# Kernel tuning notes

Hardware: AMD Instinct MI355X
Metric: run time of the kernel (lower is better)

The kernel has to match this reference:

```python
import jax, jax.numpy as jnp
import numpy as np

N_NODES = 50000
N_EDGES = 800000
IN_DIM = 64
EDGE_DIM = 32
OUT_DIM = 64
HID = IN_DIM + EDGE_DIM  # repo MLP defaults hidden width = layer input width


def setup_inputs() -> dict:
    key = jax.random.key(0)
    ks = jax.random.split(key, 7)
    x = jax.random.normal(ks[0], (N_NODES, IN_DIM), dtype=jnp.float32)
    edge_index = jax.random.randint(ks[1], (2, N_EDGES), 0, N_NODES, dtype=jnp.int64)
    edge_attr = jax.random.normal(ks[2], (N_EDGES, EDGE_DIM), dtype=jnp.float32)
    s1 = 1.0 / np.sqrt(HID)
    s2 = 1.0 / np.sqrt(HID)
    W1 = jax.random.normal(ks[3], (HID, HID), dtype=jnp.float32) * s1
    b1 = jnp.zeros((HID,), dtype=jnp.float32)
    W2 = jax.random.normal(ks[4], (HID, OUT_DIM), dtype=jnp.float32) * s2
    b2 = jnp.zeros((OUT_DIM,), dtype=jnp.float32)
    return {"x": x, "edge_index": edge_index, "edge_attr": edge_attr,
            "W1": W1, "b1": b1, "W2": W2, "b2": b2}


def reference(x, edge_index, edge_attr, W1, b1, W2, b2):
    row, col = edge_index[0], edge_index[1]
    n_nodes = x.shape[0]
    # gather source node features and fuse with edge features: [E, IN+EDGE]
    h = jnp.concatenate([x[row], edge_attr], axis=1)
    # MLP: one hidden layer with ReLU, linear output
    h = jax.nn.relu(h @ W1 + b1)
    h = h @ W2 + b2  # [E, OUT_DIM]
    # scatter_mean over destination (col) indices
    summed = jax.ops.segment_sum(h, col, num_segments=n_nodes)  # [N, OUT_DIM]
    counts = jax.ops.segment_sum(jnp.ones((h.shape[0],), dtype=h.dtype), col,
                                 num_segments=n_nodes)
    return summed / jnp.maximum(counts, 1.0)[:, None]
```

## Files before the change

### kernel.cpp

```cpp
#include <hip/hip_runtime.h>

#define N_EDGES  800000
#define N_NODES  50000
#define IN_DIM   64
#define EDGE_DIM 32
#define HID      96
#define OUT_DIM  64
#define BE       128
#define PAD      104
#define NTILES   (N_EDGES / BE)
#define THREADS  512
#define GRID     512
#define SCAN_B   1024
#define SCAN_NB  ((N_NODES + SCAN_B - 1) / SCAN_B)

typedef __attribute__((ext_vector_type(8))) short  short8;
typedef __attribute__((ext_vector_type(4))) ushort bf16x4;
typedef __attribute__((ext_vector_type(4))) float  f32x4;

__device__ inline ushort f2bf(float f) {
    union { float f; unsigned u; } v; v.f = f;
    unsigned r = v.u + 0x7FFFu + ((v.u >> 16) & 1u);
    return (ushort)(r >> 16);
}
__device__ inline float b2f(ushort u) {
    union { unsigned u; float f; } v; v.u = ((unsigned)u) << 16;
    return v.f;
}

__global__ __launch_bounds__(256) void zero_hist_kernel(int* __restrict__ hist) {
    int i = blockIdx.x * 256 + threadIdx.x;
    if (i < N_NODES) hist[i] = 0;
}

__global__ __launch_bounds__(256) void hist_kernel(const int* __restrict__ ei,
                                                   int* __restrict__ hist) {
    int e = blockIdx.x * 256 + threadIdx.x;
    if (e < N_EDGES) atomicAdd(&hist[ei[N_EDGES + e]], 1);
}

__global__ __launch_bounds__(SCAN_B) void scan1_kernel(const int* __restrict__ hist,
                                                       int* __restrict__ starts,
                                                       int* __restrict__ bsums) {
    __shared__ int buf[2][SCAN_B];
    const int tid = threadIdx.x;
    const int gid = blockIdx.x * SCAN_B + tid;
    int v = (gid < N_NODES) ? hist[gid] : 0;
    int cur = 0;
    buf[0][tid] = v;
    __syncthreads();
    #pragma unroll
    for (int off = 1; off < SCAN_B; off <<= 1) {
        int t = buf[cur][tid] + ((tid >= off) ? buf[cur][tid - off] : 0);
        buf[cur ^ 1][tid] = t;
        __syncthreads();
        cur ^= 1;
    }
    int incl = buf[cur][tid];
    if (gid < N_NODES) starts[gid] = incl;
    if (tid == SCAN_B - 1) bsums[blockIdx.x] = incl;
}

__global__ __launch_bounds__(64) void scan2_kernel(int* __restrict__ bsums) {
    if (threadIdx.x == 0) {
        int acc = 0;
        for (int i = 0; i < SCAN_NB; ++i) { int t = bsums[i]; bsums[i] = acc; acc += t; }
    }
}

__global__ __launch_bounds__(SCAN_B) void scan3_kernel(const int* __restrict__ hist,
                                                       int* __restrict__ starts,
                                                       int* __restrict__ cursor,
                                                       const int* __restrict__ bsums) {
    const int gid = blockIdx.x * SCAN_B + threadIdx.x;
    if (gid < N_NODES) {
        int e = starts[gid] - hist[gid] + bsums[blockIdx.x];
        starts[gid] = e;
        cursor[gid] = e;
    }
}

__global__ __launch_bounds__(256) void fill_kernel(const int* __restrict__ ei,
                                                   int* __restrict__ cursor,
                                                   int* __restrict__ ids) {
    int e = blockIdx.x * 256 + threadIdx.x;
    if (e < N_EDGES) {
        int c = ei[N_EDGES + e];
        int p = atomicAdd(&cursor[c], 1);
        ids[p] = e;
    }
}

__global__ __launch_bounds__(256) void zero_kernel(float* __restrict__ out,
                                                   float* __restrict__ cnt) {
    int i = blockIdx.x * 256 + threadIdx.x;
    if (i < N_NODES * OUT_DIM) out[i] = 0.0f;
    if (i < N_NODES) cnt[i] = 0.0f;
}

__global__ __launch_bounds__(256) void div_kernel(float* __restrict__ out,
                                                  const float* __restrict__ cnt) {
    int i = blockIdx.x * 256 + threadIdx.x;
    if (i < N_NODES * OUT_DIM) {
        float c = cnt[i / OUT_DIM];
        out[i] = out[i] / fmaxf(c, 1.0f);
    }
}

template <bool ATOMIC>
__global__ __launch_bounds__(THREADS, 4) void edge_mlp_mfma_kernel(
    const float* __restrict__ x,
    const int*   __restrict__ ei,
    const float* __restrict__ ea,
    const float* __restrict__ W1,
    const float* __restrict__ b1,
    const float* __restrict__ W2,
    const float* __restrict__ b2,
    float*       __restrict__ out,
    float*       __restrict__ cnt,
    ushort*      __restrict__ temp)
{
    __shared__ ushort sA[BE][PAD];
    __shared__ ushort sW1T[HID][PAD];
    __shared__ ushort sW2T[OUT_DIM][PAD];

    const int tid  = threadIdx.x;
    const int wave = tid >> 6;
    const int lane = tid & 63;
    const int lr   = lane & 15;
    const int lg   = lane >> 4;
    const int el_base = wave * 16;

    #pragma unroll 2
    for (int i = tid; i < HID * HID / 4; i += THREADS) {
        float4 v = reinterpret_cast<const float4*>(W1)[i];
        int k = (i * 4) / HID, n = (i * 4) % HID;
        sW1T[n + 0][k] = f2bf(v.x); sW1T[n + 1][k] = f2bf(v.y);
        sW1T[n + 2][k] = f2bf(v.z); sW1T[n + 3][k] = f2bf(v.w);
    }
    #pragma unroll 2
    for (int i = tid; i < HID * OUT_DIM / 4; i += THREADS) {
        float4 v = reinterpret_cast<const float4*>(W2)[i];
        int k = (i * 4) / OUT_DIM, n = (i * 4) % OUT_DIM;
        sW2T[n + 0][k] = f2bf(v.x); sW2T[n + 1][k] = f2bf(v.y);
        sW2T[n + 2][k] = f2bf(v.z); sW2T[n + 3][k] = f2bf(v.w);
    }
    float rb1[6], rb2[4];
    #pragma unroll
    for (int nt = 0; nt < 6; ++nt) rb1[nt] = b1[nt * 16 + lr];
    #pragma unroll
    for (int nt = 0; nt < 4; ++nt) rb2[nt] = b2[nt * 16 + lr];
    __syncthreads();

    for (int tl = blockIdx.x; tl < NTILES; tl += gridDim.x) {
        const int e0 = tl * BE;

        {
            const int el   = el_base + (lane >> 2);
            const int part = lane & 3;
            const int e    = e0 + el;
            const int src  = ei[e];
            const float4* xp = reinterpret_cast<const float4*>(x) + (size_t)src * 16;
            const float4* ep = reinterpret_cast<const float4*>(ea) + (size_t)e * 8;
            #pragma unroll
            for (int i = 0; i < 6; ++i) {
                const int f = part + 4 * i;
                float4 v = (i < 4) ? xp[f] : ep[f - 16];
                bf16x4 w = { f2bf(v.x), f2bf(v.y), f2bf(v.z), f2bf(v.w) };
                *(bf16x4*)&sA[el][f * 4] = w;
            }
            if constexpr (ATOMIC) {
                if (part == 0) atomicAdd(cnt + ei[N_EDGES + e], 1.0f);
            }
        }
        asm volatile("s_waitcnt lgkmcnt(0)" ::: "memory");
        __builtin_amdgcn_sched_barrier(0);

        short8 af[3];
        #pragma unroll
        for (int ks = 0; ks < 3; ++ks)
            af[ks] = *(const short8*)&sA[el_base + lr][ks * 32 + lg * 8];

        f32x4 acc1[6];
        #pragma unroll
        for (int nt = 0; nt < 6; ++nt) {
            float bv = rb1[nt];
            acc1[nt] = f32x4{ bv, bv, bv, bv };
        }
        #pragma unroll
        for (int nt = 0; nt < 6; ++nt) {
            short8 bf[3];
            #pragma unroll
            for (int ks = 0; ks < 3; ++ks)
                bf[ks] = *(const short8*)&sW1T[nt * 16 + lr][ks * 32 + lg * 8];
            #pragma unroll
            for (int ks = 0; ks < 3; ++ks)
                acc1[nt] = __builtin_amdgcn_mfma_f32_16x16x32_bf16(
                    af[ks], bf[ks], acc1[nt], 0, 0, 0);
        }

        #pragma unroll
        for (int nt = 0; nt < 6; ++nt)
            #pragma unroll
            for (int j = 0; j < 4; ++j)
                sA[el_base + lg * 4 + j][nt * 16 + lr] =
                    f2bf(fmaxf(acc1[nt][j], 0.0f));
        asm volatile("s_waitcnt lgkmcnt(0)" ::: "memory");
        __builtin_amdgcn_sched_barrier(0);

        short8 a2[3];
        #pragma unroll
        for (int ks = 0; ks < 3; ++ks)
            a2[ks] = *(const short8*)&sA[el_base + lr][ks * 32 + lg * 8];

        f32x4 acc2[4];
        #pragma unroll
        for (int nt = 0; nt < 4; ++nt) {
            float bv = rb2[nt];
            acc2[nt] = f32x4{ bv, bv, bv, bv };
        }
        #pragma unroll
        for (int nt = 0; nt < 4; ++nt) {
            short8 bf[3];
            #pragma unroll
            for (int ks = 0; ks < 3; ++ks)
                bf[ks] = *(const short8*)&sW2T[nt * 16 + lr][ks * 32 + lg * 8];
            #pragma unroll
            for (int ks = 0; ks < 3; ++ks)
                acc2[nt] = __builtin_amdgcn_mfma_f32_16x16x32_bf16(
                    a2[ks], bf[ks], acc2[nt], 0, 0, 0);
        }

        if constexpr (ATOMIC) {
            int nd[4];
            #pragma unroll
            for (int j = 0; j < 4; ++j)
                nd[j] = ei[N_EDGES + e0 + el_base + lg * 4 + j];
            #pragma unroll
            for (int nt = 0; nt < 4; ++nt)
                #pragma unroll
                for (int j = 0; j < 4; ++j)
                    atomicAdd(out + (size_t)nd[j] * OUT_DIM + nt * 16 + lr,
                              acc2[nt][j]);
        } else {
            #pragma unroll
            for (int nt = 0; nt < 4; ++nt)
                #pragma unroll
                for (int j = 0; j < 4; ++j)
                    sA[el_base + lg * 4 + j][nt * 16 + lr] = f2bf(acc2[nt][j]);
            asm volatile("s_waitcnt lgkmcnt(0)" ::: "memory");
            __builtin_amdgcn_sched_barrier(0);
            const int rr = lane >> 2, pp = lane & 3;
            ushort* dst = temp + (size_t)(e0 + el_base + rr) * OUT_DIM + pp * 16;
            short8 v0 = *(const short8*)&sA[el_base + rr][pp * 16];
            short8 v1 = *(const short8*)&sA[el_base + rr][pp * 16 + 8];
            *(short8*)dst = v0;
            *(short8*)(dst + 8) = v1;
        }
    }
}

__global__ __launch_bounds__(256) void pull_kernel(const ushort* __restrict__ temp,
                                                   const int* __restrict__ ids,
                                                   const int* __restrict__ starts,
                                                   const int* __restrict__ hist,
                                                   float* __restrict__ out) {
    const int wave = threadIdx.x >> 6;
    const int lane = threadIdx.x & 63;
    const int node = blockIdx.x * 4 + wave;
    if (node >= N_NODES) return;
    const int deg = hist[node];
    const int st  = starts[node];
    float s = 0.0f;
    int i = 0;
    for (; i + 4 <= deg; i += 4) {
        int e0 = ids[st + i], e1 = ids[st + i + 1];
        int e2 = ids[st + i + 2], e3 = ids[st + i + 3];
        float a = b2f(temp[(size_t)e0 * OUT_DIM + lane]);
        float b = b2f(temp[(size_t)e1 * OUT_DIM + lane]);
        float c = b2f(temp[(size_t)e2 * OUT_DIM + lane]);
        float d = b2f(temp[(size_t)e3 * OUT_DIM + lane]);
        s += (a + b) + (c + d);
    }
    for (; i < deg; ++i)
        s += b2f(temp[(size_t)ids[st + i] * OUT_DIM + lane]);
    out[(size_t)node * OUT_DIM + lane] = s / fmaxf((float)deg, 1.0f);
}

extern "C" void kernel_launch(void* const* d_in, const int* in_sizes, int n_in,
                              void* d_out, int out_size, void* d_ws, size_t ws_size,
                              hipStream_t stream) {
    const float* x  = (const float*)d_in[0];
    const int*   ei = (const int*)d_in[1];
    const float* ea = (const float*)d_in[2];
    const float* W1 = (const float*)d_in[3];
    const float* b1 = (const float*)d_in[4];
    const float* W2 = (const float*)d_in[5];
    const float* b2 = (const float*)d_in[6];
    float* out = (float*)d_out;

    char* ws = (char*)d_ws;
    const size_t tempB    = (size_t)N_EDGES * OUT_DIM * sizeof(ushort);
    const size_t idsOff   = tempB;
    const size_t histOff  = idsOff + (size_t)N_EDGES * 4;
    const size_t strOff   = histOff + (size_t)N_NODES * 4;
    const size_t curOff   = strOff + (size_t)N_NODES * 4;
    const size_t bsumOff  = curOff + (size_t)N_NODES * 4;
    const size_t need     = bsumOff + 64 * 4;

    if (ws_size >= need) {
        ushort* temp  = (ushort*)ws;
        int* ids      = (int*)(ws + idsOff);
        int* hist     = (int*)(ws + histOff);
        int* starts   = (int*)(ws + strOff);
        int* cursor   = (int*)(ws + curOff);
        int* bsums    = (int*)(ws + bsumOff);

        zero_hist_kernel<<<(N_NODES + 255) / 256, 256, 0, stream>>>(hist);
        hist_kernel<<<N_EDGES / 256, 256, 0, stream>>>(ei, hist);
        scan1_kernel<<<SCAN_NB, SCAN_B, 0, stream>>>(hist, starts, bsums);
        scan2_kernel<<<1, 64, 0, stream>>>(bsums);
        scan3_kernel<<<SCAN_NB, SCAN_B, 0, stream>>>(hist, starts, cursor, bsums);
        fill_kernel<<<N_EDGES / 256, 256, 0, stream>>>(ei, cursor, ids);
        edge_mlp_mfma_kernel<false><<<GRID, THREADS, 0, stream>>>(
            x, ei, ea, W1, b1, W2, b2, out, nullptr, temp);
        pull_kernel<<<(N_NODES + 3) / 4, 256, 0, stream>>>(temp, ids, starts, hist, out);
    } else {
        float* cnt = (float*)d_ws;
        zero_kernel<<<(N_NODES * OUT_DIM + 255) / 256, 256, 0, stream>>>(out, cnt);
        edge_mlp_mfma_kernel<true><<<GRID, THREADS, 0, stream>>>(
            x, ei, ea, W1, b1, W2, b2, out, cnt, nullptr);
        div_kernel<<<(N_NODES * OUT_DIM + 255) / 256, 256, 0, stream>>>(out, cnt);
    }
}
```

Measured before the change: 204.0 us.

## Process edges in destination-sorted order and fuse segmented reduction into MLP kernel

The fill kernel now writes edges into CSR order as source, edge-id and destination arrays. The MLP kernel processes edges in that order and reduces runs of equal destinations within each 16-row wave tile before issuing float atomics into the output. This removes the bf16 temp buffer round-trip and the separate pull kernel, but adds atomics, a memset of the output and a divide pass. It also folds the bsums scan into scan3 with a wave reduction, replaces the zeroing kernel with memsets, and keeps the W2 fragments in registers across tiles.

After: 250.7 us. 1.23x slower.

```diff
diff --git a/kernel.cpp b/kernel.cpp
--- a/kernel.cpp
+++ b/kernel.cpp
@@ -28,11 +28,6 @@
     return v.f;
 }
 
-__global__ __launch_bounds__(256) void zero_hist_kernel(int* __restrict__ hist) {
-    int i = blockIdx.x * 256 + threadIdx.x;
-    if (i < N_NODES) hist[i] = 0;
-}
-
 __global__ __launch_bounds__(256) void hist_kernel(const int* __restrict__ ei,
                                                    int* __restrict__ hist) {
     int e = blockIdx.x * 256 + threadIdx.x;
@@ -61,20 +56,21 @@
     if (tid == SCAN_B - 1) bsums[blockIdx.x] = incl;
 }
 
-__global__ __launch_bounds__(64) void scan2_kernel(int* __restrict__ bsums) {
-    if (threadIdx.x == 0) {
-        int acc = 0;
-        for (int i = 0; i < SCAN_NB; ++i) { int t = bsums[i]; bsums[i] = acc; acc += t; }
-    }
-}
-
 __global__ __launch_bounds__(SCAN_B) void scan3_kernel(const int* __restrict__ hist,
                                                        int* __restrict__ starts,
                                                        int* __restrict__ cursor,
                                                        const int* __restrict__ bsums) {
+    __shared__ int s_off;
+    if (threadIdx.x < 64) {
+        int v = ((int)threadIdx.x < (int)blockIdx.x) ? bsums[threadIdx.x] : 0;
+        #pragma unroll
+        for (int o = 32; o >= 1; o >>= 1) v += __shfl_xor(v, o, 64);
+        if (threadIdx.x == 0) s_off = v;
+    }
+    __syncthreads();
     const int gid = blockIdx.x * SCAN_B + threadIdx.x;
     if (gid < N_NODES) {
-        int e = starts[gid] - hist[gid] + bsums[blockIdx.x];
+        int e = starts[gid] - hist[gid] + s_off;
         starts[gid] = e;
         cursor[gid] = e;
     }
@@ -82,12 +78,16 @@
 
 __global__ __launch_bounds__(256) void fill_kernel(const int* __restrict__ ei,
                                                    int* __restrict__ cursor,
-                                                   int* __restrict__ ids) {
+                                                   int* __restrict__ srcs,
+                                                   int* __restrict__ eids,
+                                                   int* __restrict__ dsts) {
     int e = blockIdx.x * 256 + threadIdx.x;
     if (e < N_EDGES) {
         int c = ei[N_EDGES + e];
         int p = atomicAdd(&cursor[c], 1);
-        ids[p] = e;
+        srcs[p] = ei[e];
+        eids[p] = e;
+        dsts[p] = c;
     }
 }
 
@@ -107,8 +107,164 @@
     }
 }
 
-template <bool ATOMIC>
-__global__ __launch_bounds__(THREADS, 4) void edge_mlp_mfma_kernel(
+__global__ __launch_bounds__(256) void div_int_kernel(float* __restrict__ out,
+                                                      const int* __restrict__ hist) {
+    int i = blockIdx.x * 256 + threadIdx.x;
+    if (i < N_NODES * OUT_DIM) {
+        float c = (float)hist[i >> 6];
+        out[i] = out[i] / fmaxf(c, 1.0f);
+    }
+}
+
+__global__ __launch_bounds__(THREADS, 4) void edge_mlp_csr_kernel(
+    const float* __restrict__ x,
+    const float* __restrict__ ea,
+    const int*   __restrict__ srcs,
+    const int*   __restrict__ eids,
+    const int*   __restrict__ dsts,
+    const float* __restrict__ W1,
+    const float* __restrict__ b1,
+    const float* __restrict__ W2,
+    const float* __restrict__ b2,
+    float*       __restrict__ out)
+{
+    __shared__ ushort sA[BE][PAD];
+    __shared__ ushort sW1T[HID][PAD];
+    __shared__ ushort sW2T[OUT_DIM][PAD];
+
+    const int tid  = threadIdx.x;
+    const int wave = tid >> 6;
+    const int lane = tid & 63;
+    const int lr   = lane & 15;
+    const int lg   = lane >> 4;
+    const int el_base = wave * 16;
+    const int el   = el_base + (lane >> 2);
+    const int part = lane & 3;
+
+    #pragma unroll 2
+    for (int i = tid; i < HID * HID / 4; i += THREADS) {
+        float4 v = reinterpret_cast<const float4*>(W1)[i];
+        int k = (i * 4) / HID, n = (i * 4) % HID;
+        sW1T[n + 0][k] = f2bf(v.x); sW1T[n + 1][k] = f2bf(v.y);
+        sW1T[n + 2][k] = f2bf(v.z); sW1T[n + 3][k] = f2bf(v.w);
+    }
+    #pragma unroll 2
+    for (int i = tid; i < HID * OUT_DIM / 4; i += THREADS) {
+        float4 v = reinterpret_cast<const float4*>(W2)[i];
+        int k = (i * 4) / OUT_DIM, n = (i * 4) % OUT_DIM;
+        sW2T[n + 0][k] = f2bf(v.x); sW2T[n + 1][k] = f2bf(v.y);
+        sW2T[n + 2][k] = f2bf(v.z); sW2T[n + 3][k] = f2bf(v.w);
+    }
+    float rb1[6], rb2[4];
+    #pragma unroll
+    for (int nt = 0; nt < 6; ++nt) rb1[nt] = b1[nt * 16 + lr];
+    #pragma unroll
+    for (int nt = 0; nt < 4; ++nt) rb2[nt] = b2[nt * 16 + lr];
+    __syncthreads();
+
+    short8 bw2[4][3];
+    #pragma unroll
+    for (int nt = 0; nt < 4; ++nt)
+        #pragma unroll
+        for (int ks = 0; ks < 3; ++ks)
+            bw2[nt][ks] = *(const short8*)&sW2T[nt * 16 + lr][ks * 32 + lg * 8];
+
+    for (int tl = blockIdx.x; tl < NTILES; tl += GRID) {
+        const int e0 = tl * BE;
+
+        {
+            const int slot = e0 + el;
+            const int src  = srcs[slot];
+            const int eid  = eids[slot];
+            const float4* xp = reinterpret_cast<const float4*>(x) + (size_t)src * 16;
+            const float4* ep = reinterpret_cast<const float4*>(ea) + (size_t)eid * 8;
+            #pragma unroll
+            for (int i = 0; i < 6; ++i) {
+                const int f = part + 4 * i;
+                float4 v = (i < 4) ? xp[f] : ep[f - 16];
+                bf16x4 w = { f2bf(v.x), f2bf(v.y), f2bf(v.z), f2bf(v.w) };
+                *(bf16x4*)&sA[el][f * 4] = w;
+            }
+        }
+        int dreg[17];
+        #pragma unroll
+        for (int r = 0; r < 16; ++r) dreg[r] = dsts[e0 + el_base + r];
+        dreg[16] = -1;
+
+        asm volatile("s_waitcnt lgkmcnt(0)" ::: "memory");
+        __builtin_amdgcn_sched_barrier(0);
+
+        short8 af[3];
+        #pragma unroll
+        for (int ks = 0; ks < 3; ++ks)
+            af[ks] = *(const short8*)&sA[el_base + lr][ks * 32 + lg * 8];
+
+        f32x4 acc1[6];
+        #pragma unroll
+        for (int nt = 0; nt < 6; ++nt) {
+            float bv = rb1[nt];
+            acc1[nt] = f32x4{ bv, bv, bv, bv };
+        }
+        #pragma unroll
+        for (int nt = 0; nt < 6; ++nt) {
+            short8 bf[3];
+            #pragma unroll
+            for (int ks = 0; ks < 3; ++ks)
+                bf[ks] = *(const short8*)&sW1T[nt * 16 + lr][ks * 32 + lg * 8];
+            #pragma unroll
+            for (int ks = 0; ks < 3; ++ks)
+                acc1[nt] = __builtin_amdgcn_mfma_f32_16x16x32_bf16(
+                    af[ks], bf[ks], acc1[nt], 0, 0, 0);
+        }
+
+        #pragma unroll
+        for (int nt = 0; nt < 6; ++nt)
+            #pragma unroll
+            for (int j = 0; j < 4; ++j)
+                sA[el_base + lg * 4 + j][nt * 16 + lr] =
+                    f2bf(fmaxf(acc1[nt][j], 0.0f));
+        asm volatile("s_waitcnt lgkmcnt(0)" ::: "memory");
+        __builtin_amdgcn_sched_barrier(0);
+
+        short8 a2[3];
+        #pragma unroll
+        for (int ks = 0; ks < 3; ++ks)
+            a2[ks] = *(const short8*)&sA[el_base + lr][ks * 32 + lg * 8];
+
+        f32x4 acc2[4];
+        #pragma unroll
+        for (int nt = 0; nt < 4; ++nt) {
+            float bv = rb2[nt];
+            acc2[nt] = f32x4{ bv, bv, bv, bv };
+        }
+        #pragma unroll
+        for (int nt = 0; nt < 4; ++nt)
+            #pragma unroll
+            for (int ks = 0; ks < 3; ++ks)
+                acc2[nt] = __builtin_amdgcn_mfma_f32_16x16x32_bf16(
+                    a2[ks], bw2[nt][ks], acc2[nt], 0, 0, 0);
+
+        #pragma unroll
+        for (int nt = 0; nt < 4; ++nt)
+            #pragma unroll
+            for (int j = 0; j < 4; ++j)
+                sA[el_base + lg * 4 + j][nt * 16 + lr] = f2bf(acc2[nt][j]);
+        asm volatile("s_waitcnt lgkmcnt(0)" ::: "memory");
+        __builtin_amdgcn_sched_barrier(0);
+
+        float s = 0.0f;
+        #pragma unroll
+        for (int r = 0; r < 16; ++r) {
+            s += b2f(sA[el_base + r][lane]);
+            if (r == 15 || dreg[r + 1] != dreg[r]) {
+                atomicAdd(out + (size_t)dreg[r] * OUT_DIM + lane, s);
+                s = 0.0f;
+            }
+        }
+    }
+}
+
+__global__ __launch_bounds__(THREADS, 4) void edge_mlp_atomic_kernel(
     const float* __restrict__ x,
     const int*   __restrict__ ei,
     const float* __restrict__ ea,
@@ -117,8 +273,7 @@
     const float* __restrict__ W2,
     const float* __restrict__ b2,
     float*       __restrict__ out,
-    float*       __restrict__ cnt,
-    ushort*      __restrict__ temp)
+    float*       __restrict__ cnt)
 {
     __shared__ ushort sA[BE][PAD];
     __shared__ ushort sW1T[HID][PAD];
@@ -130,6 +285,8 @@
     const int lr   = lane & 15;
     const int lg   = lane >> 4;
     const int el_base = wave * 16;
+    const int el   = el_base + (lane >> 2);
+    const int part = lane & 3;
 
     #pragma unroll 2
     for (int i = tid; i < HID * HID / 4; i += THREADS) {
@@ -152,14 +309,18 @@
     for (int nt = 0; nt < 4; ++nt) rb2[nt] = b2[nt * 16 + lr];
     __syncthreads();
 
-    for (int tl = blockIdx.x; tl < NTILES; tl += gridDim.x) {
+    short8 bw2[4][3];
+    #pragma unroll
+    for (int nt = 0; nt < 4; ++nt)
+        #pragma unroll
+        for (int ks = 0; ks < 3; ++ks)
+            bw2[nt][ks] = *(const short8*)&sW2T[nt * 16 + lr][ks * 32 + lg * 8];
+
+    for (int tl = blockIdx.x; tl < NTILES; tl += GRID) {
         const int e0 = tl * BE;
-
         {
-            const int el   = el_base + (lane >> 2);
-            const int part = lane & 3;
-            const int e    = e0 + el;
-            const int src  = ei[e];
+            const int e   = e0 + el;
+            const int src = ei[e];
             const float4* xp = reinterpret_cast<const float4*>(x) + (size_t)src * 16;
             const float4* ep = reinterpret_cast<const float4*>(ea) + (size_t)e * 8;
             #pragma unroll
@@ -169,9 +330,7 @@
                 bf16x4 w = { f2bf(v.x), f2bf(v.y), f2bf(v.z), f2bf(v.w) };
                 *(bf16x4*)&sA[el][f * 4] = w;
             }
-            if constexpr (ATOMIC) {
-                if (part == 0) atomicAdd(cnt + ei[N_EDGES + e], 1.0f);
-            }
+            if (part == 0) atomicAdd(cnt + ei[N_EDGES + e], 1.0f);
         }
         asm volatile("s_waitcnt lgkmcnt(0)" ::: "memory");
         __builtin_amdgcn_sched_barrier(0);
@@ -180,7 +339,6 @@
         #pragma unroll
         for (int ks = 0; ks < 3; ++ks)
             af[ks] = *(const short8*)&sA[el_base + lr][ks * 32 + lg * 8];
-
         f32x4 acc1[6];
         #pragma unroll
         for (int nt = 0; nt < 6; ++nt) {
@@ -198,7 +356,6 @@
                 acc1[nt] = __builtin_amdgcn_mfma_f32_16x16x32_bf16(
                     af[ks], bf[ks], acc1[nt], 0, 0, 0);
         }
-
         #pragma unroll
         for (int nt = 0; nt < 6; ++nt)
             #pragma unroll
@@ -212,7 +369,6 @@
         #pragma unroll
         for (int ks = 0; ks < 3; ++ks)
             a2[ks] = *(const short8*)&sA[el_base + lr][ks * 32 + lg * 8];
-
         f32x4 acc2[4];
         #pragma unroll
         for (int nt = 0; nt < 4; ++nt) {
@@ -220,71 +376,23 @@
             acc2[nt] = f32x4{ bv, bv, bv, bv };
         }
         #pragma unroll
-        for (int nt = 0; nt < 4; ++nt) {
-            short8 bf[3];
-            #pragma unroll
-            for (int ks = 0; ks < 3; ++ks)
-                bf[ks] = *(const short8*)&sW2T[nt * 16 + lr][ks * 32 + lg * 8];
+        for (int nt = 0; nt < 4; ++nt)
             #pragma unroll
             for (int ks = 0; ks < 3; ++ks)
                 acc2[nt] = __builtin_amdgcn_mfma_f32_16x16x32_bf16(
-                    a2[ks], bf[ks], acc2[nt], 0, 0, 0);
-        }
-
-        if constexpr (ATOMIC) {
-            int nd[4];
+                    a2[ks], bw2[nt][ks], acc2[nt], 0, 0, 0);
+
+        int nd[4];
+        #pragma unroll
+        for (int j = 0; j < 4; ++j)
+            nd[j] = ei[N_EDGES + e0 + el_base + lg * 4 + j];
+        #pragma unroll
+        for (int nt = 0; nt < 4; ++nt)
             #pragma unroll
             for (int j = 0; j < 4; ++j)
-                nd[j] = ei[N_EDGES + e0 + el_base + lg * 4 + j];
-            #pragma unroll
-            for (int nt = 0; nt < 4; ++nt)
-                #pragma unroll
-                for (int j = 0; j < 4; ++j)
-                    atomicAdd(out + (size_t)nd[j] * OUT_DIM + nt * 16 + lr,
-                              acc2[nt][j]);
-        } else {
-            #pragma unroll
-            for (int nt = 0; nt < 4; ++nt)
-                #pragma unroll
-                for (int j = 0; j < 4; ++j)
-                    sA[el_base + lg * 4 + j][nt * 16 + lr] = f2bf(acc2[nt][j]);
-            asm volatile("s_waitcnt lgkmcnt(0)" ::: "memory");
-            __builtin_amdgcn_sched_barrier(0);
-            const int rr = lane >> 2, pp = lane & 3;
-            ushort* dst = temp + (size_t)(e0 + el_base + rr) * OUT_DIM + pp * 16;
-            short8 v0 = *(const short8*)&sA[el_base + rr][pp * 16];
-            short8 v1 = *(const short8*)&sA[el_base + rr][pp * 16 + 8];
-            *(short8*)dst = v0;
-            *(short8*)(dst + 8) = v1;
-        }
-    }
-}
-
-__global__ __launch_bounds__(256) void pull_kernel(const ushort* __restrict__ temp,
-                                                   const int* __restrict__ ids,
-                                                   const int* __restrict__ starts,
-                                                   const int* __restrict__ hist,
-                                                   float* __restrict__ out) {
-    const int wave = threadIdx.x >> 6;
-    const int lane = threadIdx.x & 63;
-    const int node = blockIdx.x * 4 + wave;
-    if (node >= N_NODES) return;
-    const int deg = hist[node];
-    const int st  = starts[node];
-    float s = 0.0f;
-    int i = 0;
-    for (; i + 4 <= deg; i += 4) {
-        int e0 = ids[st + i], e1 = ids[st + i + 1];
-        int e2 = ids[st + i + 2], e3 = ids[st + i + 3];
-        float a = b2f(temp[(size_t)e0 * OUT_DIM + lane]);
-        float b = b2f(temp[(size_t)e1 * OUT_DIM + lane]);
-        float c = b2f(temp[(size_t)e2 * OUT_DIM + lane]);
-        float d = b2f(temp[(size_t)e3 * OUT_DIM + lane]);
-        s += (a + b) + (c + d);
-    }
-    for (; i < deg; ++i)
-        s += b2f(temp[(size_t)ids[st + i] * OUT_DIM + lane]);
-    out[(size_t)node * OUT_DIM + lane] = s / fmaxf((float)deg, 1.0f);
+                atomicAdd(out + (size_t)nd[j] * OUT_DIM + nt * 16 + lr,
+                          acc2[nt][j]);
+    }
 }
 
 extern "C" void kernel_launch(void* const* d_in, const int* in_sizes, int n_in,
@@ -300,36 +408,38 @@
     float* out = (float*)d_out;
 
     char* ws = (char*)d_ws;
-    const size_t tempB    = (size_t)N_EDGES * OUT_DIM * sizeof(ushort);
-    const size_t idsOff   = tempB;
-    const size_t histOff  = idsOff + (size_t)N_EDGES * 4;
-    const size_t strOff   = histOff + (size_t)N_NODES * 4;
-    const size_t curOff   = strOff + (size_t)N_NODES * 4;
-    const size_t bsumOff  = curOff + (size_t)N_NODES * 4;
-    const size_t need     = bsumOff + 64 * 4;
+    const size_t srcsOff = 0;
+    const size_t eidsOff = srcsOff + (size_t)N_EDGES * 4;
+    const size_t dstsOff = eidsOff + (size_t)N_EDGES * 4;
+    const size_t histOff = dstsOff + (size_t)N_EDGES * 4;
+    const size_t strOff  = histOff + (size_t)N_NODES * 4;
+    const size_t curOff  = strOff + (size_t)N_NODES * 4;
+    const size_t bsumOff = curOff + (size_t)N_NODES * 4;
+    const size_t need    = bsumOff + 64 * 4;
 
     if (ws_size >= need) {
-        ushort* temp  = (ushort*)ws;
-        int* ids      = (int*)(ws + idsOff);
-        int* hist     = (int*)(ws + histOff);
-        int* starts   = (int*)(ws + strOff);
-        int* cursor   = (int*)(ws + curOff);
-        int* bsums    = (int*)(ws + bsumOff);
-
-        zero_hist_kernel<<<(N_NODES + 255) / 256, 256, 0, stream>>>(hist);
+        int* srcs   = (int*)(ws + srcsOff);
+        int* eids   = (int*)(ws + eidsOff);
+        int* dsts   = (int*)(ws + dstsOff);
+        int* hist   = (int*)(ws + histOff);
+        int* starts = (int*)(ws + strOff);
+        int* cursor = (int*)(ws + curOff);
+        int* bsums  = (int*)(ws + bsumOff);
+
+        hipMemsetAsync(hist, 0, (size_t)N_NODES * 4, stream);
+        hipMemsetAsync(out, 0, (size_t)N_NODES * OUT_DIM * 4, stream);
         hist_kernel<<<N_EDGES / 256, 256, 0, stream>>>(ei, hist);
         scan1_kernel<<<SCAN_NB, SCAN_B, 0, stream>>>(hist, starts, bsums);
-        scan2_kernel<<<1, 64, 0, stream>>>(bsums);
         scan3_kernel<<<SCAN_NB, SCAN_B, 0, stream>>>(hist, starts, cursor, bsums);
-        fill_kernel<<<N_EDGES / 256, 256, 0, stream>>>(ei, cursor, ids);
-        edge_mlp_mfma_kernel<false><<<GRID, THREADS, 0, stream>>>(
-            x, ei, ea, W1, b1, W2, b2, out, nullptr, temp);
-        pull_kernel<<<(N_NODES + 3) / 4, 256, 0, stream>>>(temp, ids, starts, hist, out);
+        fill_kernel<<<N_EDGES / 256, 256, 0, stream>>>(ei, cursor, srcs, eids, dsts);
+        edge_mlp_csr_kernel<<<GRID, THREADS, 0, stream>>>(
+            x, ea, srcs, eids, dsts, W1, b1, W2, b2, out);
+        div_int_kernel<<<(N_NODES * OUT_DIM + 255) / 256, 256, 0, stream>>>(out, hist);
     } else {
         float* cnt = (float*)d_ws;
         zero_kernel<<<(N_NODES * OUT_DIM + 255) / 256, 256, 0, stream>>>(out, cnt);
-        edge_mlp_mfma_kernel<true><<<GRID, THREADS, 0, stream>>>(
-            x, ei, ea, W1, b1, W2, b2, out, cnt, nullptr);
+        edge_mlp_atomic_kernel<<<GRID, THREADS, 0, stream>>>(
+            x, ei, ea, W1, b1, W2, b2, out, cnt);
         div_kernel<<<(N_NODES * OUT_DIM + 255) / 256, 256, 0, stream>>>(out, cnt);
     }
 }
```
